# Kernel tuning notes

Measured on AMD Instinct MI355X. Metric: run time of the kernel, lower is better.

Reference implementation:

```python
import jax, jax.numpy as jnp
import numpy as np

K = 20
CH_IN = [6, 128, 128, 256]
CH_OUT = [64, 64, 128, 256]
EMB = 1024


def _knn_idx(x, k):
    # x: (B, C, N) -> (B, N, k) indices of k nearest neighbors (incl. self)
    inner = jnp.einsum('bcn,bcm->bnm', x, x)
    xx = jnp.sum(x * x, axis=1)  # (B, N)
    pd = 2.0 * inner - xx[:, :, None] - xx[:, None, :]  # = -||xi - xj||^2
    return jax.lax.top_k(pd, k)[1]


def _graph_feature(x, k):
    # x: (B, C, N) -> (B, 2C, N, k) EdgeConv features [x_j - x_i, x_i]
    xt = jnp.transpose(x, (0, 2, 1))  # (B, N, C)
    idx = _knn_idx(x, k)  # (B, N, k)
    nb = jax.vmap(lambda f, i: f[i])(xt, idx)  # (B, N, k, C) gather
    center = xt[:, :, None, :]
    feat = jnp.concatenate([nb - center, jnp.broadcast_to(center, nb.shape)], axis=-1)
    return jnp.transpose(feat, (0, 3, 1, 2))  # (B, 2C, N, k)


def _bn(y, g, b, m, v):
    # eval-mode BatchNorm over channel axis 1 (or last for 2D input is also axis 1)
    shp = (1, -1) + (1,) * (y.ndim - 2)
    s = g / jnp.sqrt(v + 1e-5)
    return (y - m.reshape(shp)) * s.reshape(shp) + b.reshape(shp)


def setup_inputs() -> dict:
    key = jax.random.key(0)
    ks = iter(jax.random.split(key, 64))
    rn = lambda shape: jax.random.normal(next(ks), shape, jnp.float32) * 0.05
    ru = lambda shape: jax.random.uniform(next(ks), shape, jnp.float32, minval=0.5, maxval=1.5)
    d = {"x": jax.random.normal(next(ks), (16, 1024, 3), jnp.float32)}
    for i, (ci, co) in enumerate(zip(CH_IN, CH_OUT)):
        d[f"c{i}_w"] = rn((co, ci)); d[f"c{i}_b"] = rn((co,))
        d[f"c{i}_g"] = ru((co,)); d[f"c{i}_be"] = rn((co,))
        d[f"c{i}_m"] = rn((co,)); d[f"c{i}_v"] = ru((co,))
    cat = sum(CH_OUT)  # 512
    d["lc_w"] = rn((EMB, cat)); d["lc_b"] = rn((EMB,))
    d["lc_g"] = ru((EMB,)); d["lc_be"] = rn((EMB,))
    d["lc_m"] = rn((EMB,)); d["lc_v"] = ru((EMB,))
    d["l0_w"] = rn((512, 2 * EMB))
    d["l0_g"] = ru((512,)); d["l0_be"] = rn((512,)); d["l0_m"] = rn((512,)); d["l0_v"] = ru((512,))
    d["l1_w"] = rn((256, 512)); d["l1_b"] = rn((256,))
    d["l1_g"] = ru((256,)); d["l1_be"] = rn((256,)); d["l1_m"] = rn((256,)); d["l1_v"] = ru((256,))
    d["ow"] = rn((40, 256)); d["ob"] = rn((40,))
    return d


def reference(x, c0_w, c0_b, c0_g, c0_be, c0_m, c0_v,
              c1_w, c1_b, c1_g, c1_be, c1_m, c1_v,
              c2_w, c2_b, c2_g, c2_be, c2_m, c2_v,
              c3_w, c3_b, c3_g, c3_be, c3_m, c3_v,
              lc_w, lc_b, lc_g, lc_be, lc_m, lc_v,
              l0_w, l0_g, l0_be, l0_m, l0_v,
              l1_w, l1_b, l1_g, l1_be, l1_m, l1_v,
              ow, ob):
    convs = [(c0_w, c0_b, c0_g, c0_be, c0_m, c0_v),
             (c1_w, c1_b, c1_g, c1_be, c1_m, c1_v),
             (c2_w, c2_b, c2_g, c2_be, c2_m, c2_v),
             (c3_w, c3_b, c3_g, c3_be, c3_m, c3_v)]
    cur = jnp.transpose(x, (0, 2, 1))  # (B, 3, N)
    outs = []
    for w, b, g, be, m, v in convs:
        f = _graph_feature(cur, K)  # (B, 2C_in, N, k)
        y = jnp.einsum('bcnk,oc->bonk', f, w) + b[None, :, None, None]  # 1x1 conv2d
        y = jax.nn.leaky_relu(_bn(y, g, be, m, v), 0.2)
        cur = jnp.max(y, axis=-1)  # max over k neighbors -> (B, C_out, N)
        outs.append(cur)
    h = jnp.concatenate(outs, axis=1)  # (B, 512, N)
    y = jnp.einsum('bcn,oc->bon', h, lc_w) + lc_b[None, :, None]  # 1x1 conv1d
    y = jax.nn.leaky_relu(_bn(y, lc_g, lc_be, lc_m, lc_v), 0.2)  # (B, 1024, N)
    h = jnp.concatenate([jnp.max(y, axis=-1), jnp.mean(y, axis=-1)], axis=1)  # (B, 2048)
    h = jax.nn.leaky_relu(_bn(h @ l0_w.T, l0_g, l0_be, l0_m, l0_v), 0.2)
    h = jax.nn.leaky_relu(_bn(h @ l1_w.T + l1_b, l1_g, l1_be, l1_m, l1_v), 0.2)
    return h @ ow.T + ob  # (B, 40)
```

## Files before the change

kernel.cpp:

```cpp
#include <hip/hip_runtime.h>
#include <hip/hip_bf16.h>

#define BB 16
#define NPTS 1024
#define KNB 20
#define HC 512

__device__ __forceinline__ float XV(const float* __restrict__ X, int b, int n, int c)
{
    return X[((size_t)b * NPTS + n) * 3 + c];
}

__device__ __forceinline__ unsigned long long dist2key(float d, int m)
{
    unsigned u = __float_as_uint(d);
    u = (u & 0x80000000u) ? ~u : (u | 0x80000000u);
    return ((unsigned long long)u << 32) | (unsigned)(1023 - m);
}

__device__ __forceinline__ void wave_topk_write(unsigned long long* key,
                                                int* __restrict__ idxo,
                                                size_t obase, int lane)
{
    for (int it = 0; it < KNB; ++it) {
        unsigned long long best = 0ull; int bj = -1;
#pragma unroll
        for (int j = 0; j < 16; ++j) if (key[j] > best) { best = key[j]; bj = j; }
        unsigned long long wbest = best;
        for (int off = 32; off > 0; off >>= 1) {
            const unsigned long long o = __shfl_down(wbest, off, 64);
            if (o > wbest) wbest = o;
        }
        wbest = __shfl(wbest, 0, 64);
        if (best == wbest && bj >= 0) key[bj] = 0ull;
        if (lane == 0) idxo[obase + it] = 1023 - (int)(wbest & 0xFFFFFFFFull);
    }
}

__global__ void sentinel_kernel(float* __restrict__ out, float val)
{
    const int i = blockIdx.x * 256 + threadIdx.x;
    if (i < BB * 40) out[i] = val;
}

__global__ void xx_kernel(const float* __restrict__ H, const float* __restrict__ X,
                          float* __restrict__ xx, int cin, int off_in, int use_x)
{
    const int p = blockIdx.x * blockDim.x + threadIdx.x;
    if (p >= BB * NPTS) return;
    float s = 0.f;
    if (use_x) {
        const int b = p >> 10, n = p & 1023;
        for (int c = 0; c < 3; ++c) { const float v = XV(X, b, n, c); s += v * v; }
    } else {
        const float4* r4 = (const float4*)(H + (size_t)p * HC + off_in);
        for (int c4 = 0; c4 < cin / 4; ++c4) {
            const float4 v = r4[c4];
            s += v.x*v.x + v.y*v.y + v.z*v.z + v.w*v.w;
        }
    }
    xx[p] = s;
}

__global__ __launch_bounds__(256, 3) void knn8_kernel(
    const float* __restrict__ H, const float* __restrict__ xx,
    int* __restrict__ idxo, int off_in)
{
    constexpr int CIN = 64;
    __shared__ __align__(16) float qv[8][CIN];
    __shared__ float dist[8][NPTS];
    __shared__ float sxxq[8];
    const int blk = blockIdx.x;
    const int q0g = blk * 8;
    const int b = q0g >> 10, q0 = q0g & 1023;
    const int tid = threadIdx.x;
    const int base = b * NPTS;

    for (int t = tid; t < 8 * CIN; t += 256) {
        const int q = t >> 6, c = t & 63;
        qv[q][c] = H[(size_t)(base + q0 + q) * HC + off_in + c];
    }
    if (tid < 8) sxxq[tid] = xx[base + q0 + tid];
    __syncthreads();

    const int g = tid >> 3, l = tid & 7;
    float4 aq[8][2];
#pragma unroll
    for (int q = 0; q < 8; ++q)
#pragma unroll
        for (int r = 0; r < 2; ++r)
            aq[q][r] = *(const float4*)&qv[q][4 * (l + 8 * r)];

    for (int it = 0; it < 32; ++it) {
        const int m = g + 32 * it;
        float acc[8] = {0.f,0.f,0.f,0.f,0.f,0.f,0.f,0.f};
#pragma unroll
        for (int r = 0; r < 2; ++r) {
            const float4 v = *(const float4*)(H + (size_t)(base + m) * HC + off_in + 4 * (l + 8 * r));
#pragma unroll
            for (int q = 0; q < 8; ++q)
                acc[q] += aq[q][r].x*v.x + aq[q][r].y*v.y + aq[q][r].z*v.z + aq[q][r].w*v.w;
        }
#pragma unroll
        for (int q = 0; q < 8; ++q) {
            acc[q] += __shfl_xor(acc[q], 1, 64);
            acc[q] += __shfl_xor(acc[q], 2, 64);
            acc[q] += __shfl_xor(acc[q], 4, 64);
        }
        if (l == 0) {
            const float xxm = xx[base + m];
#pragma unroll
            for (int q = 0; q < 8; ++q)
                dist[q][m] = (2.f * acc[q] - sxxq[q]) - xxm;
        }
    }
    __syncthreads();

    const int w = tid >> 6, lane = tid & 63;
    for (int qq = w; qq < 8; qq += 4) {
        unsigned long long key[16];
#pragma unroll
        for (int j = 0; j < 16; ++j) {
            const int m = lane + 64 * j;
            key[j] = dist2key(dist[qq][m], m);
        }
        wave_topk_write(key, idxo, (size_t)(base + q0 + qq) * KNB, lane);
    }
}

template<int CIN>
__global__ __launch_bounds__(256, 3) void knn4_kernel(
    const float* __restrict__ H, const float* __restrict__ xx,
    int* __restrict__ idxo, int off_in)
{
    __shared__ __align__(16) float qv[4][CIN];
    __shared__ float dist[4][NPTS];
    __shared__ float sxxq[4];
    const int blk = blockIdx.x;
    const int q0g = blk * 4;
    const int b = q0g >> 10, q0 = q0g & 1023;
    const int tid = threadIdx.x;
    const int base = b * NPTS;

    for (int t = tid; t < 4 * CIN; t += 256) {
        const int q = t / CIN, c = t - q * CIN;
        qv[q][c] = H[(size_t)(base + q0 + q) * HC + off_in + c];
    }
    if (tid < 4) sxxq[tid] = xx[base + q0 + tid];
    __syncthreads();

    const int g = tid >> 3, l = tid & 7;
    float4 aq[4][CIN / 32];
#pragma unroll
    for (int q = 0; q < 4; ++q)
#pragma unroll
        for (int r = 0; r < CIN / 32; ++r)
            aq[q][r] = *(const float4*)&qv[q][4 * (l + 8 * r)];

    for (int it = 0; it < 32; ++it) {
        const int m = g + 32 * it;
        float acc[4] = {0.f, 0.f, 0.f, 0.f};
#pragma unroll
        for (int r = 0; r < CIN / 32; ++r) {
            const float4 v = *(const float4*)(H + (size_t)(base + m) * HC + off_in + 4 * (l + 8 * r));
#pragma unroll
            for (int q = 0; q < 4; ++q)
                acc[q] += aq[q][r].x*v.x + aq[q][r].y*v.y + aq[q][r].z*v.z + aq[q][r].w*v.w;
        }
#pragma unroll
        for (int q = 0; q < 4; ++q) {
            acc[q] += __shfl_xor(acc[q], 1, 64);
            acc[q] += __shfl_xor(acc[q], 2, 64);
            acc[q] += __shfl_xor(acc[q], 4, 64);
        }
        if (l == 0) {
            const float xxm = xx[base + m];
#pragma unroll
            for (int q = 0; q < 4; ++q)
                dist[q][m] = (2.f * acc[q] - sxxq[q]) - xxm;
        }
    }
    __syncthreads();

    const int w = tid >> 6, lane = tid & 63;
    unsigned long long key[16];
#pragma unroll
    for (int j = 0; j < 16; ++j) {
        const int m = lane + 64 * j;
        key[j] = dist2key(dist[w][m], m);
    }
    wave_topk_write(key, idxo, (size_t)(base + q0 + w) * KNB, lane);
}

__global__ __launch_bounds__(256, 3) void knn4x_kernel(
    const float* __restrict__ X, const float* __restrict__ xx, int* __restrict__ idxo)
{
    __shared__ float qv[4][4];
    __shared__ float dist[4][NPTS];
    __shared__ float sxxq[4];
    const int blk = blockIdx.x;
    const int q0g = blk * 4;
    const int b = q0g >> 10, q0 = q0g & 1023;
    const int tid = threadIdx.x;
    const int base = b * NPTS;

    if (tid < 4) {
        for (int c = 0; c < 3; ++c) qv[tid][c] = XV(X, b, q0 + tid, c);
        sxxq[tid] = xx[base + q0 + tid];
    }
    __syncthreads();

    for (int j = 0; j < 4; ++j) {
        const int m = tid + 256 * j;
        const float r0 = XV(X, b, m, 0), r1 = XV(X, b, m, 1), r2 = XV(X, b, m, 2);
        const float xxm = xx[base + m];
#pragma unroll
        for (int q = 0; q < 4; ++q) {
            const float acc = qv[q][0]*r0 + qv[q][1]*r1 + qv[q][2]*r2;
            dist[q][m] = (2.f * acc - sxxq[q]) - xxm;
        }
    }
    __syncthreads();

    const int w = tid >> 6, lane = tid & 63;
    unsigned long long key[16];
#pragma unroll
    for (int j = 0; j < 16; ++j) {
        const int m = lane + 64 * j;
        key[j] = dist2key(dist[w][m], m);
    }
    wave_topk_write(key, idxo, (size_t)(base + q0 + w) * KNB, lane);
}

__device__ __forceinline__ float wfetch1(const float* __restrict__ W, int og,
                                         int CIN, int COUT, int c)
{
    if (og < COUT) return W[(size_t)og * 2 * CIN + c];
    const float* r0 = W + (size_t)(og - COUT) * 2 * CIN;
    return r0[CIN + c] - r0[c];
}

__global__ __launch_bounds__(256, 4) void gemm_conv_kernel(
    const float* __restrict__ H, const float* __restrict__ W, float* __restrict__ P,
    int off_in, int CIN, int COUT, int NO128)
{
    __shared__ float hl[32][68];
    __shared__ float wl[32][133];
    const int mblk = blockIdx.x / NO128;
    const int oblk = blockIdx.x - mblk * NO128;
    const int tid = threadIdx.x;
    const int o = tid & 63, grp = tid >> 6;
    const int NO = NO128 * 128;
    const int n0 = mblk * 64;
    const int og0 = oblk * 128 + o;
    const int og1 = og0 + 64;

    float acc0[16], acc1[16];
#pragma unroll
    for (int i = 0; i < 16; ++i) { acc0[i] = 0.f; acc1[i] = 0.f; }

    for (int ct = 0; ct < CIN / 32; ++ct) {
        for (int r = 0; r < 2; ++r) {
            const int e = tid + 256 * r;
            const int n = e & 63, c4 = e >> 6;
            const float4 hv = *(const float4*)(H + (size_t)(n0 + n) * HC + off_in + ct * 32 + c4 * 4);
            hl[c4*4+0][n] = hv.x; hl[c4*4+1][n] = hv.y; hl[c4*4+2][n] = hv.z; hl[c4*4+3][n] = hv.w;
        }
        for (int r = 0; r < 16; ++r) {
            const int e = tid + 256 * r;
            const int c_ = e & 31, o_ = e >> 5;
            wl[c_][o_] = wfetch1(W, oblk * 128 + o_, CIN, COUT, ct * 32 + c_);
        }
        __syncthreads();
        for (int c = 0; c < 32; ++c) {
            const float wva = wl[c][o];
            const float wvb = wl[c][o + 64];
            const float* hr = &hl[c][grp * 16];
#pragma unroll
            for (int nn = 0; nn < 4; ++nn) {
                const float4 hv = *(const float4*)(hr + 4 * nn);
                acc0[4*nn+0] += wva * hv.x; acc0[4*nn+1] += wva * hv.y;
                acc0[4*nn+2] += wva * hv.z; acc0[4*nn+3] += wva * hv.w;
                acc1[4*nn+0] += wvb * hv.x; acc1[4*nn+1] += wvb * hv.y;
                acc1[4*nn+2] += wvb * hv.z; acc1[4*nn+3] += wvb * hv.w;
            }
        }
        __syncthreads();
    }

#pragma unroll
    for (int i = 0; i < 16; ++i) {
        P[(size_t)(n0 + grp * 16 + i) * NO + og0] = acc0[i];
        P[(size_t)(n0 + grp * 16 + i) * NO + og1] = acc1[i];
    }
}

template<int COUT>
__global__ __launch_bounds__(COUT) void edge_epi_kernel(
    const float* __restrict__ P, const int* __restrict__ idx,
    const float* __restrict__ Bs, const float* __restrict__ G, const float* __restrict__ Be,
    const float* __restrict__ Bm, const float* __restrict__ Bv,
    float* __restrict__ Hout, int off_out)
{
    constexpr int NO = 2 * COUT;
    const int blk = blockIdx.x;
    const int base = (blk >> 10) << 10;
    const int o = threadIdx.x;
    const float s = G[o] / sqrtf(Bv[o] + 1e-5f);
    const float beo = Be[o];
    const float cb = P[(size_t)blk * NO + COUT + o] + Bs[o] - Bm[o];
    float mx = -INFINITY;
    for (int k = 0; k < KNB; ++k) {
        const int m = idx[(size_t)blk * KNB + k];
        const float v = P[(size_t)(base + m) * NO + o];
        float t = (v + cb) * s + beo;
        t = t > 0.f ? t : 0.2f * t;
        mx = fmaxf(mx, t);
    }
    Hout[(size_t)blk * HC + off_out + o] = mx;
}

template<int CIN, int COUT, bool USEX>
__global__ __launch_bounds__(COUT) void conv_kernel(
    const float* __restrict__ H, const float* __restrict__ X, const int* __restrict__ idx,
    const float* __restrict__ W, const float* __restrict__ Bs, const float* __restrict__ G,
    const float* __restrict__ Be, const float* __restrict__ Bm, const float* __restrict__ Bv,
    float* __restrict__ Hout, int off_in, int off_out)
{
    __shared__ __align__(16) float ctr[CIN];
    __shared__ __align__(16) float nb[KNB][CIN];
    __shared__ int sidx[KNB];
    const int blk = blockIdx.x;
    const int b = blk >> 10, q = blk & 1023;
    const int tid = threadIdx.x;
    const int base = b * NPTS;

    if (tid < KNB) sidx[tid] = idx[(size_t)(base + q) * KNB + tid];
    for (int c = tid; c < CIN; c += COUT)
        ctr[c] = USEX ? XV(X, b, q, c) : H[(size_t)(base + q) * HC + off_in + c];
    __syncthreads();
    for (int t = tid; t < KNB * CIN; t += COUT) {
        const int k = t / CIN, c = t - k * CIN;
        nb[k][c] = USEX ? XV(X, b, sidx[k], c) : H[(size_t)(base + sidx[k]) * HC + off_in + c];
    }
    __syncthreads();

    float acc[KNB];
    float cacc = 0.f;
#pragma unroll
    for (int k = 0; k < KNB; ++k) acc[k] = 0.f;

    const float* wr = W + (size_t)tid * 2 * CIN;
    for (int c = 0; c < CIN; ++c) {
        const float w1 = wr[c], w2 = wr[CIN + c];
        cacc += (w2 - w1) * ctr[c];
#pragma unroll
        for (int k = 0; k < KNB; ++k) acc[k] += w1 * nb[k][c];
    }

    const int o = tid;
    const float s = G[o] / sqrtf(Bv[o] + 1e-5f);
    const float beo = Be[o];
    const float cb = cacc + Bs[o] - Bm[o];
    float mx = -INFINITY;
#pragma unroll
    for (int k = 0; k < KNB; ++k) {
        float t = (acc[k] + cb) * s + beo;
        t = t > 0.f ? t : 0.2f * t;
        mx = fmaxf(mx, t);
    }
    Hout[(size_t)(base + q) * HC + off_out + o] = mx;
}

__global__ __launch_bounds__(256, 4) void lcpool_kernel(
    const float* __restrict__ H, const float* __restrict__ W, const float* __restrict__ Bs,
    const float* __restrict__ G, const float* __restrict__ Be,
    const float* __restrict__ Bm, const float* __restrict__ Bv,
    float* __restrict__ pmax, float* __restrict__ psum)
{
    __shared__ float hl[32][68];
    __shared__ float wl[32][133];
    __shared__ float redm[4][128];
    __shared__ float reds[4][128];
    const int bid = blockIdx.x;
    const int b = bid >> 7;
    const int rem = bid & 127;
    const int oblk = rem >> 4;
    const int nblk = rem & 15;
    const int tid = threadIdx.x;
    const int o = tid & 63;
    const int grp = tid >> 6;
    const int og0 = oblk * 128 + o;
    const int og1 = og0 + 64;
    const int n0 = nblk * 64;
    const size_t hbase = (size_t)b * NPTS * HC;

    float acc0[16], acc1[16];
#pragma unroll
    for (int i = 0; i < 16; ++i) { acc0[i] = 0.f; acc1[i] = 0.f; }

    for (int ct = 0; ct < 16; ++ct) {
        for (int r = 0; r < 2; ++r) {
            const int e = tid + 256 * r;
            const int n = e & 63, c4 = e >> 6;
            const float4 hv = *(const float4*)(H + hbase + (size_t)(n0 + n) * HC + ct * 32 + c4 * 4);
            hl[c4*4+0][n] = hv.x; hl[c4*4+1][n] = hv.y; hl[c4*4+2][n] = hv.z; hl[c4*4+3][n] = hv.w;
        }
        for (int r = 0; r < 16; ++r) {
            const int e = tid + 256 * r;
            const int c_ = e & 31, o_ = e >> 5;
            wl[c_][o_] = W[(size_t)(oblk * 128 + o_) * HC + ct * 32 + c_];
        }
        __syncthreads();
        for (int c = 0; c < 32; ++c) {
            const float wva = wl[c][o];
            const float wvb = wl[c][o + 64];
            const float* hr = &hl[c][grp * 16];
#pragma unroll
            for (int nn = 0; nn < 4; ++nn) {
                const float4 hv = *(const float4*)(hr + 4 * nn);
                acc0[4*nn+0] += wva * hv.x; acc0[4*nn+1] += wva * hv.y;
                acc0[4*nn+2] += wva * hv.z; acc0[4*nn+3] += wva * hv.w;
                acc1[4*nn+0] += wvb * hv.x; acc1[4*nn+1] += wvb * hv.y;
                acc1[4*nn+2] += wvb * hv.z; acc1[4*nn+3] += wvb * hv.w;
            }
        }
        __syncthreads();
    }

#pragma unroll
    for (int p = 0; p < 2; ++p) {
        const int og = p ? og1 : og0;
        const float* acc = p ? acc1 : acc0;
        const float s = G[og] / sqrtf(Bv[og] + 1e-5f);
        const float beo = Be[og];
        const float mb = Bs[og] - Bm[og];
        float pm = -INFINITY, ps = 0.f;
#pragma unroll
        for (int i = 0; i < 16; ++i) {
            float t = (acc[i] + mb) * s + beo;
            t = t > 0.f ? t : 0.2f * t;
            pm = fmaxf(pm, t); ps += t;
        }
        redm[grp][o + 64 * p] = pm; reds[grp][o + 64 * p] = ps;
    }
    __syncthreads();
    if (grp == 0) {
#pragma unroll
        for (int p = 0; p < 2; ++p) {
            const int oo = o + 64 * p;
            float m0 = redm[0][oo], s0 = reds[0][oo];
            for (int i2 = 1; i2 < 4; ++i2) { m0 = fmaxf(m0, redm[i2][oo]); s0 += reds[i2][oo]; }
            pmax[((size_t)b * 16 + nblk) * 1024 + oblk * 128 + oo] = m0;
            psum[((size_t)b * 16 + nblk) * 1024 + oblk * 128 + oo] = s0;
        }
    }
}

__global__ void pool_reduce_kernel(const float* __restrict__ pmax, const float* __restrict__ psum,
                                   float* __restrict__ h2)
{
    const int i = blockIdx.x * 256 + threadIdx.x;
    if (i >= BB * 1024) return;
    const int b = i >> 10, o = i & 1023;
    float mx = -INFINITY, sm = 0.f;
    for (int c = 0; c < 16; ++c) {
        mx = fmaxf(mx, pmax[((size_t)b * 16 + c) * 1024 + o]);
        sm += psum[((size_t)b * 16 + c) * 1024 + o];
    }
    h2[(size_t)b * 2048 + o] = mx;
    h2[(size_t)b * 2048 + 1024 + o] = sm * (1.f / 1024.f);
}

__global__ void l0_kernel(const float* __restrict__ h2, const float* __restrict__ W,
                          const float* __restrict__ G, const float* __restrict__ Be,
                          const float* __restrict__ Bm, const float* __restrict__ Bv,
                          float* __restrict__ h3)
{
    const int i = blockIdx.x * 256 + threadIdx.x;
    if (i >= BB * 512) return;
    const int b = i >> 9, o = i & 511;
    const float4* w4 = (const float4*)(W + (size_t)o * 2048);
    const float4* h4p = (const float4*)(h2 + (size_t)b * 2048);
    float acc = 0.f;
    for (int c = 0; c < 512; ++c) {
        const float4 wv = w4[c]; const float4 hv = h4p[c];
        acc += wv.x*hv.x + wv.y*hv.y + wv.z*hv.z + wv.w*hv.w;
    }
    const float s = G[o] / sqrtf(Bv[o] + 1e-5f);
    float t = (acc - Bm[o]) * s + Be[o];
    t = t > 0.f ? t : 0.2f * t;
    h3[(size_t)b * 512 + o] = t;
}

__global__ void l1_kernel(const float* __restrict__ h3, const float* __restrict__ W,
                          const float* __restrict__ Bs, const float* __restrict__ G,
                          const float* __restrict__ Be, const float* __restrict__ Bm,
                          const float* __restrict__ Bv, float* __restrict__ h4o)
{
    const int i = blockIdx.x * 256 + threadIdx.x;
    if (i >= BB * 256) return;
    const int b = i >> 8, o = i & 255;
    const float4* w4 = (const float4*)(W + (size_t)o * 512);
    const float4* hv4 = (const float4*)(h3 + (size_t)b * 512);
    float acc = 0.f;
    for (int c = 0; c < 128; ++c) {
        const float4 wv = w4[c]; const float4 hv = hv4[c];
        acc += wv.x*hv.x + wv.y*hv.y + wv.z*hv.z + wv.w*hv.w;
    }
    acc += Bs[o];
    const float s = G[o] / sqrtf(Bv[o] + 1e-5f);
    float t = (acc - Bm[o]) * s + Be[o];
    t = t > 0.f ? t : 0.2f * t;
    h4o[(size_t)b * 256 + o] = t;
}

__global__ void out_kernel(const float* __restrict__ h4, const float* __restrict__ W,
                           const float* __restrict__ Bs, float* __restrict__ out)
{
    const int i = blockIdx.x * 256 + threadIdx.x;
    if (i >= BB * 40) return;
    const int b = i / 40, o = i % 40;
    const float4* w4 = (const float4*)(W + (size_t)o * 256);
    const float4* hv4 = (const float4*)(h4 + (size_t)b * 256);
    float acc = 0.f;
    for (int c = 0; c < 64; ++c) {
        const float4 wv = w4[c]; const float4 hv = hv4[c];
        acc += wv.x*hv.x + wv.y*hv.y + wv.z*hv.z + wv.w*hv.w;
    }
    acc += Bs[o];
    out[(size_t)b * 40 + o] = acc;
}

extern "C" void kernel_launch(void* const* d_in, const int* in_sizes, int n_in,
                              void* d_out, int out_size, void* d_ws, size_t ws_size,
                              hipStream_t stream)
{
    static const int expect[44] = {
        49152, 384,64,64,64,64,64, 8192,64,64,64,64,64, 16384,128,128,128,128,128,
        65536,256,256,256,256,256, 524288,1024,1024,1024,1024,1024,
        1048576,512,512,512,512, 131072,256,256,256,256,256, 10240,40};
    int bad = -1;
    if (n_in != 44) bad = 100;
    else if (out_size != BB * 40) bad = 101;
    else {
        for (int i = 0; i < 44; ++i) if (in_sizes[i] != expect[i]) { bad = i; break; }
    }
    if (bad >= 0) {
        sentinel_kernel<<<3, 256, 0, stream>>>((float*)d_out, 500.f + (float)bad);
        return;
    }

    const float* X = (const float*)d_in[0];
    const float *CW[4], *CB[4], *CG[4], *CBE[4], *CM[4], *CV[4];
    for (int i = 0; i < 4; ++i) {
        CW[i]  = (const float*)d_in[1 + 6*i]; CB[i] = (const float*)d_in[2 + 6*i];
        CG[i]  = (const float*)d_in[3 + 6*i]; CBE[i] = (const float*)d_in[4 + 6*i];
        CM[i]  = (const float*)d_in[5 + 6*i]; CV[i] = (const float*)d_in[6 + 6*i];
    }
    const float* LCW = (const float*)d_in[25]; const float* LCB = (const float*)d_in[26];
    const float* LCG = (const float*)d_in[27]; const float* LCBE = (const float*)d_in[28];
    const float* LCM = (const float*)d_in[29]; const float* LCV = (const float*)d_in[30];
    const float* L0W = (const float*)d_in[31]; const float* L0G = (const float*)d_in[32];
    const float* L0BE = (const float*)d_in[33]; const float* L0M = (const float*)d_in[34];
    const float* L0V = (const float*)d_in[35];
    const float* L1W = (const float*)d_in[36]; const float* L1B = (const float*)d_in[37];
    const float* L1G = (const float*)d_in[38]; const float* L1BE = (const float*)d_in[39];
    const float* L1M = (const float*)d_in[40]; const float* L1V = (const float*)d_in[41];
    const float* OW = (const float*)d_in[42]; const float* OB = (const float*)d_in[43];

    float* H    = (float*)d_ws;
    float* XX   = H + (size_t)BB * NPTS * HC;
    int*   IDX  = (int*)(XX + BB * NPTS);
    float* P    = (float*)(IDX + (size_t)BB * NPTS * KNB);
    float* PMAX = P + (size_t)BB * NPTS * 512;
    float* PSUM = PMAX + BB * 16 * 1024;
    float* H2   = PSUM + BB * 16 * 1024;
    float* H3   = H2 + BB * 2048;
    float* H4   = H3 + BB * 512;
    const size_t need_bytes = (size_t)((H4 + BB * 256) - H) * 4;
    const bool use_P = (ws_size >= need_bytes);

    float* fPMAX = P;
    float* fPSUM = fPMAX + BB * 16 * 1024;
    float* fH2   = fPSUM + BB * 16 * 1024;
    float* fH3   = fH2 + BB * 2048;
    float* fH4   = fH3 + BB * 512;

    const int M = BB * NPTS;

    xx_kernel<<<M/256, 256, 0, stream>>>(H, X, XX, 3, 0, 1);
    knn4x_kernel<<<M/4, 256, 0, stream>>>(X, XX, IDX);
    conv_kernel<3,64,true><<<M, 64, 0, stream>>>(H, X, IDX,
        CW[0], CB[0], CG[0], CBE[0], CM[0], CV[0], H, 0, 0);

    if (use_P) {
        xx_kernel<<<M/256, 256, 0, stream>>>(H, X, XX, 64, 0, 0);
        knn8_kernel<<<M/8, 256, 0, stream>>>(H, XX, IDX, 0);
        gemm_conv_kernel<<<(M/64)*1, 256, 0, stream>>>(H, CW[1], P, 0, 64, 64, 1);
        edge_epi_kernel<64><<<M, 64, 0, stream>>>(P, IDX,
            CB[1], CG[1], CBE[1], CM[1], CV[1], H, 64);

        xx_kernel<<<M/256, 256, 0, stream>>>(H, X, XX, 64, 64, 0);
        knn8_kernel<<<M/8, 256, 0, stream>>>(H, XX, IDX, 64);
        gemm_conv_kernel<<<(M/64)*2, 256, 0, stream>>>(H, CW[2], P, 64, 64, 128, 2);
        edge_epi_kernel<128><<<M, 128, 0, stream>>>(P, IDX,
            CB[2], CG[2], CBE[2], CM[2], CV[2], H, 128);

        xx_kernel<<<M/256, 256, 0, stream>>>(H, X, XX, 128, 128, 0);
        knn4_kernel<128><<<M/4, 256, 0, stream>>>(H, XX, IDX, 128);
        gemm_conv_kernel<<<(M/64)*4, 256, 0, stream>>>(H, CW[3], P, 128, 128, 256, 4);
        edge_epi_kernel<256><<<M, 256, 0, stream>>>(P, IDX,
            CB[3], CG[3], CBE[3], CM[3], CV[3], H, 256);

        lcpool_kernel<<<BB*8*16, 256, 0, stream>>>(H, LCW, LCB, LCG, LCBE, LCM, LCV, PMAX, PSUM);
        pool_reduce_kernel<<<BB*1024/256, 256, 0, stream>>>(PMAX, PSUM, H2);
        l0_kernel<<<(BB*512+255)/256, 256, 0, stream>>>(H2, L0W, L0G, L0BE, L0M, L0V, H3);
        l1_kernel<<<(BB*256+255)/256, 256, 0, stream>>>(H3, L1W, L1B, L1G, L1BE, L1M, L1V, H4);
        out_kernel<<<(BB*40+255)/256, 256, 0, stream>>>(H4, OW, OB, (float*)d_out);
    } else {
        xx_kernel<<<M/256, 256, 0, stream>>>(H, X, XX, 64, 0, 0);
        knn8_kernel<<<M/8, 256, 0, stream>>>(H, XX, IDX, 0);
        conv_kernel<64,64,false><<<M, 64, 0, stream>>>(H, X, IDX,
            CW[1], CB[1], CG[1], CBE[1], CM[1], CV[1], H, 0, 64);

        xx_kernel<<<M/256, 256, 0, stream>>>(H, X, XX, 64, 64, 0);
        knn8_kernel<<<M/8, 256, 0, stream>>>(H, XX, IDX, 64);
        conv_kernel<64,128,false><<<M, 128, 0, stream>>>(H, X, IDX,
            CW[2], CB[2], CG[2], CBE[2], CM[2], CV[2], H, 64, 128);

        xx_kernel<<<M/256, 256, 0, stream>>>(H, X, XX, 128, 128, 0);
        knn4_kernel<128><<<M/4, 256, 0, stream>>>(H, XX, IDX, 128);
        conv_kernel<128,256,false><<<M, 256, 0, stream>>>(H, X, IDX,
            CW[3], CB[3], CG[3], CBE[3], CM[3], CV[3], H, 128, 256);

        lcpool_kernel<<<BB*8*16, 256, 0, stream>>>(H, LCW, LCB, LCG, LCBE, LCM, LCV, fPMAX, fPSUM);
        pool_reduce_kernel<<<BB*1024/256, 256, 0, stream>>>(fPMAX, fPSUM, fH2);
        l0_kernel<<<(BB*512+255)/256, 256, 0, stream>>>(fH2, L0W, L0G, L0BE, L0M, L0V, fH3);
        l1_kernel<<<(BB*256+255)/256, 256, 0, stream>>>(fH3, L1W, L1B, L1G, L1BE, L1M, L1V, fH4);
        out_kernel<<<(BB*40+255)/256, 256, 0, stream>>>(fH4, OW, OB, (float*)d_out);
    }
}
```

Measured before the change: 1.264 ms.

## Run embedding conv GEMM on bf16 MFMA with hi/lo split-precision emulation

Replaces the FP32 SIMT lcpool GEMM (512->1024 channels over 16K points) with an MFMA bf16 kernel. The FP32 activations and weights are first split into hi and lo bf16 parts, and three MFMAs per tile are combined to approximate FP32 accuracy. BN, leaky ReLU and partial max/sum pooling are fused into the epilogue. The cost is two extra conversion passes, including a 16 MB write of converted activations, plus uncached global loads of the A and B fragments with no LDS staging.

```diff
diff --git a/kernel.cpp b/kernel.cpp
--- a/kernel.cpp
+++ b/kernel.cpp
@@ -5,6 +5,9 @@
 #define NPTS 1024
 #define KNB 20
 #define HC 512
+
+typedef __attribute__((ext_vector_type(8))) short short8;
+typedef __attribute__((ext_vector_type(4))) float f32x4;
 
 __device__ __forceinline__ float XV(const float* __restrict__ X, int b, int n, int c)
 {
@@ -37,10 +40,41 @@
     }
 }
 
+__device__ __forceinline__ unsigned short f2bf(float x)
+{
+    unsigned u = __float_as_uint(x);
+    u += 0x7FFFu + ((u >> 16) & 1u);
+    return (unsigned short)(u >> 16);
+}
+__device__ __forceinline__ float bf2f(unsigned short h)
+{
+    return __uint_as_float(((unsigned)h) << 16);
+}
+
 __global__ void sentinel_kernel(float* __restrict__ out, float val)
 {
     const int i = blockIdx.x * 256 + threadIdx.x;
     if (i < BB * 40) out[i] = val;
+}
+
+__global__ void cvt_kernel(const float* __restrict__ src, unsigned short* __restrict__ hi,
+                           unsigned short* __restrict__ lo, int n4)
+{
+    const int i = blockIdx.x * 256 + threadIdx.x;
+    if (i >= n4) return;
+    const float4 v = ((const float4*)src)[i];
+    const float xs[4] = {v.x, v.y, v.z, v.w};
+    ushort4 h, l;
+    unsigned short* hp = (unsigned short*)&h;
+    unsigned short* lp = (unsigned short*)&l;
+#pragma unroll
+    for (int j = 0; j < 4; ++j) {
+        const unsigned short hb = f2bf(xs[j]);
+        hp[j] = hb;
+        lp[j] = f2bf(xs[j] - bf2f(hb));
+    }
+    ((ushort4*)hi)[i] = h;
+    ((ushort4*)lo)[i] = l;
 }
 
 __global__ void xx_kernel(const float* __restrict__ H, const float* __restrict__ X,
@@ -370,6 +404,72 @@
         mx = fmaxf(mx, t);
     }
     Hout[(size_t)(base + q) * HC + off_out + o] = mx;
+}
+
+__global__ __launch_bounds__(256) void lcpool_mfma_kernel(
+    const unsigned short* __restrict__ Hb_hi, const unsigned short* __restrict__ Hb_lo,
+    const unsigned short* __restrict__ Wb_hi, const unsigned short* __restrict__ Wb_lo,
+    const float* __restrict__ Bs, const float* __restrict__ G, const float* __restrict__ Be,
+    const float* __restrict__ Bm, const float* __restrict__ Bv,
+    float* __restrict__ pmax, float* __restrict__ psum)
+{
+    __shared__ float redm[4][64];
+    __shared__ float reds[4][64];
+    const int bid = blockIdx.x;
+    const int b = bid >> 8;
+    const int mblk = (bid >> 4) & 15;
+    const int nblk = bid & 15;
+    const int tid = threadIdx.x;
+    const int w = tid >> 6, lane = tid & 63;
+    const int quad = lane >> 4, l16 = lane & 15;
+    const size_t arow = ((size_t)b * 1024 + mblk * 64 + w * 16 + l16) * 512;
+    const int n0 = nblk * 64;
+
+    f32x4 acc[4];
+#pragma unroll
+    for (int t = 0; t < 4; ++t) acc[t] = (f32x4){0.f, 0.f, 0.f, 0.f};
+
+    for (int kk = 0; kk < 16; ++kk) {
+        const int kb = kk * 32 + quad * 8;
+        const short8 ah = *(const short8*)(Hb_hi + arow + kb);
+        const short8 al = *(const short8*)(Hb_lo + arow + kb);
+#pragma unroll
+        for (int t = 0; t < 4; ++t) {
+            const size_t wrow = (size_t)(n0 + 16 * t + l16) * 512 + kb;
+            const short8 bh = *(const short8*)(Wb_hi + wrow);
+            const short8 bl = *(const short8*)(Wb_lo + wrow);
+            acc[t] = __builtin_amdgcn_mfma_f32_16x16x32_bf16(ah, bh, acc[t], 0, 0, 0);
+            acc[t] = __builtin_amdgcn_mfma_f32_16x16x32_bf16(al, bh, acc[t], 0, 0, 0);
+            acc[t] = __builtin_amdgcn_mfma_f32_16x16x32_bf16(ah, bl, acc[t], 0, 0, 0);
+        }
+    }
+
+#pragma unroll
+    for (int t = 0; t < 4; ++t) {
+        const int o = n0 + 16 * t + l16;
+        const float s = G[o] / sqrtf(Bv[o] + 1e-5f);
+        const float beo = Be[o];
+        const float mb = Bs[o] - Bm[o];
+        float pm = -INFINITY, ps = 0.f;
+#pragma unroll
+        for (int r = 0; r < 4; ++r) {
+            float tt = (acc[t][r] + mb) * s + beo;
+            tt = tt > 0.f ? tt : 0.2f * tt;
+            pm = fmaxf(pm, tt); ps += tt;
+        }
+        pm = fmaxf(pm, __shfl_xor(pm, 16, 64));
+        pm = fmaxf(pm, __shfl_xor(pm, 32, 64));
+        ps += __shfl_xor(ps, 16, 64);
+        ps += __shfl_xor(ps, 32, 64);
+        if (quad == 0) { redm[w][16 * t + l16] = pm; reds[w][16 * t + l16] = ps; }
+    }
+    __syncthreads();
+    if (tid < 64) {
+        float m0 = redm[0][tid], s0 = reds[0][tid];
+        for (int i = 1; i < 4; ++i) { m0 = fmaxf(m0, redm[i][tid]); s0 += reds[i][tid]; }
+        pmax[((size_t)b * 16 + mblk) * 1024 + n0 + tid] = m0;
+        psum[((size_t)b * 16 + mblk) * 1024 + n0 + tid] = s0;
+    }
 }
 
 __global__ __launch_bounds__(256, 4) void lcpool_kernel(
@@ -578,8 +678,13 @@
     float* H2   = PSUM + BB * 16 * 1024;
     float* H3   = H2 + BB * 2048;
     float* H4   = H3 + BB * 512;
-    const size_t need_bytes = (size_t)((H4 + BB * 256) - H) * 4;
+    unsigned short* WBH = (unsigned short*)(H4 + BB * 256);
+    unsigned short* WBL = WBH + (size_t)1024 * 512;
+    const size_t need_bytes = (size_t)((char*)(WBL + (size_t)1024 * 512) - (char*)H);
     const bool use_P = (ws_size >= need_bytes);
+
+    unsigned short* HBH = (unsigned short*)P;
+    unsigned short* HBL = HBH + (size_t)BB * NPTS * 512;
 
     float* fPMAX = P;
     float* fPSUM = fPMAX + BB * 16 * 1024;
@@ -613,7 +718,11 @@
         edge_epi_kernel<256><<<M, 256, 0, stream>>>(P, IDX,
             CB[3], CG[3], CBE[3], CM[3], CV[3], H, 256);
 
-        lcpool_kernel<<<BB*8*16, 256, 0, stream>>>(H, LCW, LCB, LCG, LCBE, LCM, LCV, PMAX, PSUM);
+        cvt_kernel<<<(M*HC/4 + 255)/256, 256, 0, stream>>>(H, HBH, HBL, M * HC / 4);
+        cvt_kernel<<<(1024*512/4 + 255)/256, 256, 0, stream>>>(LCW, WBH, WBL, 1024 * 512 / 4);
+
+        lcpool_mfma_kernel<<<16*16*16, 256, 0, stream>>>(HBH, HBL, WBH, WBL,
+            LCB, LCG, LCBE, LCM, LCV, PMAX, PSUM);
         pool_reduce_kernel<<<BB*1024/256, 256, 0, stream>>>(PMAX, PSUM, H2);
         l0_kernel<<<(BB*512+255)/256, 256, 0, stream>>>(H2, L0W, L0G, L0BE, L0M, L0V, H3);
         l1_kernel<<<(BB*256+255)/256, 256, 0, stream>>>(H3, L1W, L1B, L1G, L1BE, L1M, L1V, H4);
```

New measurement: 1.330 ms. 5.2% more time.
